# Kernel tuning notes

Measured on AMD Instinct MI355X. Metric: run time of the kernel, lower is better.

## Reference

```python
import jax, jax.numpy as jnp
import numpy as np

QK_K = 256      # super-block size
N_SUB = 8       # sub-blocks per super-block
SUB_SIZE = QK_K // N_SUB  # 32
NMAX_4BIT = 15.0


def _quantize_scales_6bit(scales):
    # scales: (B, N_SUB). Quantize to 6-bit grid [0..63] and dequantize; STE for grads.
    s_min = scales.min(axis=-1, keepdims=True)
    s_max = scales.max(axis=-1, keepdims=True)
    s_range = jnp.maximum(s_max - s_min, 1e-8)
    s_int = jnp.clip(jnp.round((scales - s_min) / s_range * 63.0), 0.0, 63.0)
    s_dequant = s_int / 63.0 * s_range + s_min
    return scales + jax.lax.stop_gradient(s_dequant - scales)


def fake_quantize_q4_k_m(weight):
    orig_shape = weight.shape
    w = weight.reshape(-1)
    pad = (-w.size) % QK_K
    if pad:
        w = jnp.concatenate([w, jnp.zeros((pad,), dtype=w.dtype)])
    # (n_blocks, N_SUB, SUB_SIZE)
    w_sub = w.reshape(-1, N_SUB, SUB_SIZE)
    sub_min = jnp.minimum(w_sub.min(axis=-1), 0.0)   # clamp(max=0)
    sub_max = jnpum if False else jnp.maximum(w_sub.max(axis=-1), 0.0)  # clamp(min=0)
    scale_raw = jnp.maximum(sub_max - sub_min, 1e-8) / NMAX_4BIT
    scale = _quantize_scales_6bit(scale_raw)         # (n_blocks, N_SUB)
    # super-block min, rounded through fp16 with STE
    super_min_raw = sub_min.min(axis=-1, keepdims=True)  # (n_blocks, 1)
    super_min_f16 = super_min_raw.astype(jnp.float16).astype(w.dtype)
    super_min = super_min_raw + jax.lax.stop_gradient(super_min_f16 - super_min_raw)
    adj_min = sub_min - super_min                    # (n_blocks, N_SUB)
    scale_bc = jnp.maximum(scale, 1e-8)[..., None]   # (n_blocks, N_SUB, 1)
    w_int = (w_sub - super_min[..., None] - adj_min[..., None]) / scale_bc
    w_int = jnp.clip(jnp.round(w_int), 0.0, NMAX_4BIT)
    w_dequant = w_int * scale_bc + adj_min[..., None] + super_min[..., None]
    w_out = w_sub + jax.lax.stop_gradient(w_dequant - w_sub)  # STE
    w_flat = w_out.reshape(-1)
    if pad:
        w_flat = w_flat[:-pad]
    return w_flat.reshape(orig_shape)


def setup_inputs() -> dict:
    key = jax.random.key(0)
    k1, k2, k3 = jax.random.split(key, 3)
    x = jax.random.normal(k1, (2, 2048, 4096), dtype=jnp.float32)
    weight = jax.random.normal(k2, (4096, 4096), dtype=jnp.float32) * 0.02
    bias = jax.random.normal(k3, (4096,), dtype=jnp.float32)
    return {"x": x, "weight": weight, "bias": bias}


def reference(x, weight, bias):
    # _qmode = True path: fake-quantize weight to Q4_K_M grid, then dense linear.
    fq_weight = fake_quantize_q4_k_m(weight)
    return jnp.einsum('bsd,od->bso', x, fq_weight) + bias
```

## Files before the change

### kernel.cpp

```cpp
#include <hip/hip_runtime.h>
#include <hip/hip_bf16.h>
#include <hip/hip_fp16.h>


typedef __attribute__((ext_vector_type(8))) short bf16x8;
typedef __attribute__((ext_vector_type(8))) unsigned short ushort8;
typedef __attribute__((ext_vector_type(4))) float f32x4;

__device__ __forceinline__ unsigned short f2bf(float f) {
  unsigned int u = __float_as_uint(f);
  u += 0x7fffu + ((u >> 16) & 1u);
  return (unsigned short)(u >> 16);
}

__global__ __launch_bounds__(256) void prep_kernel(
    const float* __restrict__ x, unsigned short* __restrict__ xb,
    const float* __restrict__ w, unsigned short* __restrict__ wq,
    int castBlocks) {
  if ((int)blockIdx.x < castBlocks) {
    const size_t i = ((size_t)blockIdx.x * 256 + threadIdx.x) * 8;
    const float4 a = *(const float4*)(x + i);
    const float4 b = *(const float4*)(x + i + 4);
    ushort8 o = {f2bf(a.x), f2bf(a.y), f2bf(a.z), f2bf(a.w),
                 f2bf(b.x), f2bf(b.y), f2bf(b.z), f2bf(b.w)};
    *(ushort8*)(xb + i) = o;
    return;
  }
  const int qb   = blockIdx.x - castBlocks;
  const int lane = threadIdx.x & 63;
  const int wv   = threadIdx.x >> 6;
  const size_t base = (((size_t)qb * 4 + wv) * 256) + (size_t)lane * 4;
  const float4 v = *(const float4*)(w + base);

  float mn = fminf(fminf(v.x, v.y), fminf(v.z, v.w));
  float mx = fmaxf(fmaxf(v.x, v.y), fmaxf(v.z, v.w));
#pragma unroll
  for (int off = 1; off <= 4; off <<= 1) {
    mn = fminf(mn, __shfl_xor(mn, off));
    mx = fmaxf(mx, __shfl_xor(mx, off));
  }
  const float sub_min = fminf(mn, 0.0f);
  const float sub_max = fmaxf(mx, 0.0f);
  const float scale_raw = fmaxf(sub_max - sub_min, 1e-8f) / 15.0f;

  float smn = scale_raw, smx = scale_raw, supermin = sub_min;
#pragma unroll
  for (int off = 8; off <= 32; off <<= 1) {
    smn = fminf(smn, __shfl_xor(smn, off));
    smx = fmaxf(smx, __shfl_xor(smx, off));
    supermin = fminf(supermin, __shfl_xor(supermin, off));
  }
  const float s_range = fmaxf(smx - smn, 1e-8f);
  float s_int = rintf((scale_raw - smn) / s_range * 63.0f);
  s_int = fminf(fmaxf(s_int, 0.0f), 63.0f);
  float scale = s_int / 63.0f * s_range + smn;
  scale = fmaxf(scale, 1e-8f);
  const float inv_scale = 1.0f / scale;

  const float sm  = __half2float(__float2half(supermin));
  const float adj = sub_min - sm;

  float e[4] = {v.x, v.y, v.z, v.w};
  ushort4 o;
  unsigned short* op = (unsigned short*)&o;
#pragma unroll
  for (int k = 0; k < 4; ++k) {
    const float t = (e[k] - sm) - adj;
    float qv = rintf(t * inv_scale);
    qv = fminf(fmaxf(qv, 0.0f), 15.0f);
    op[k] = f2bf((qv * scale + adj) + sm);
  }
  *(ushort4*)(wq + base) = o;
}

#define BM 256
#define BN 128
#define BK 64

__device__ __forceinline__ void async_cp16(void* lds, const void* g) {
  __builtin_amdgcn_global_load_lds(
      (__attribute__((address_space(1))) void*)(void*)g,
      (__attribute__((address_space(3))) void*)lds, 16, 0, 0);
}

__global__ __launch_bounds__(256, 2) void gemm_bt_kernel(
    const unsigned short* __restrict__ A,
    const unsigned short* __restrict__ B,
    const float* __restrict__ bias,
    float* __restrict__ C,
    int M, int N, int K) {
  __shared__ unsigned short lds_a[BM * BK];
  __shared__ unsigned short lds_b[BN * BK];

  const int tid  = threadIdx.x;
  const int lane = tid & 63;
  const int wv   = tid >> 6;
  const int wm   = wv >> 1;
  const int wn   = wv & 1;
  const int bx   = blockIdx.x;
  const int by   = blockIdx.y;

  const int rloc = tid >> 3;
  const int csw  = (tid & 7) ^ (rloc & 7);
  const int koff = csw * 8;

  const unsigned short* gA[8];
  const unsigned short* gB[4];
#pragma unroll
  for (int j = 0; j < 8; ++j)
    gA[j] = A + (size_t)(by * BM + j * 32 + rloc) * K + koff;
#pragma unroll
  for (int j = 0; j < 4; ++j)
    gB[j] = B + (size_t)(bx * BN + j * 32 + rloc) * K + koff;

  f32x4 acc[8][4] = {};

  const int arow   = wm * 128 + (lane & 15);
  const int brow   = wn * 64 + (lane & 15);
  const int kslot0 = (((lane >> 4) ^ (lane & 7))) * 8;
  const int kslot1 = kslot0 ^ 32;

  for (int k0 = 0; k0 < K; k0 += BK) {
#pragma unroll
    for (int j = 0; j < 8; ++j)
      async_cp16(lds_a + j * 2048 + tid * 8, gA[j] + k0);
#pragma unroll
    for (int j = 0; j < 4; ++j)
      async_cp16(lds_b + j * 2048 + tid * 8, gB[j] + k0);
    __syncthreads();

#pragma unroll
    for (int h = 0; h < 2; ++h) {
      const int ks = h ? kslot1 : kslot0;
      bf16x8 af[8], bfr[4];
#pragma unroll
      for (int i = 0; i < 8; ++i)
        af[i] = *(const bf16x8*)(lds_a + (arow + i * 16) * BK + ks);
#pragma unroll
      for (int j = 0; j < 4; ++j)
        bfr[j] = *(const bf16x8*)(lds_b + (brow + j * 16) * BK + ks);

#pragma unroll
      for (int i = 0; i < 8; ++i)
#pragma unroll
        for (int j = 0; j < 4; ++j)
          acc[i][j] = __builtin_amdgcn_mfma_f32_16x16x32_bf16(af[i], bfr[j],
                                                              acc[i][j], 0, 0, 0);
    }
    __syncthreads();
  }

  const int rbase = by * BM + wm * 128 + (lane >> 4) * 4;
  const int cbase = bx * BN + wn * 64 + (lane & 15);
#pragma unroll
  for (int j = 0; j < 4; ++j) {
    const int c = cbase + j * 16;
    const float bv = bias[c];
#pragma unroll
    for (int i = 0; i < 8; ++i) {
#pragma unroll
      for (int r = 0; r < 4; ++r) {
        C[(size_t)(rbase + i * 16 + r) * N + c] = acc[i][j][r] + bv;
      }
    }
  }
}

extern "C" void kernel_launch(void* const* d_in, const int* in_sizes, int n_in,
                              void* d_out, int out_size, void* d_ws, size_t ws_size,
                              hipStream_t stream) {
  const float* x    = (const float*)d_in[0];
  const float* w    = (const float*)d_in[1];
  const float* bias = (const float*)d_in[2];
  float* out = (float*)d_out;

  const long long xn = in_sizes[0];
  const long long wn = in_sizes[1];
  const int N = in_sizes[2];
  const int K = (int)(wn / N);
  const int M = (int)(xn / K);

  unsigned short* xb = (unsigned short*)d_ws;
  unsigned short* wb = xb + (size_t)M * K;

  const int castBlocks  = (int)(xn / (256 * 8));
  const int quantBlocks = (int)(wn / (256 * 4));
  prep_kernel<<<castBlocks + quantBlocks, 256, 0, stream>>>(x, xb, w, wb,
                                                            castBlocks);
  gemm_bt_kernel<<<dim3(N / BN, M / BM), 256, 0, stream>>>(xb, wb, bias, out,
                                                           M, N, K);
}
```

Measured before the change: 289.0 us.

## Double-buffer A tile in LDS and load B fragments directly from global

The A tile is double-buffered in LDS, with the next K-step prefetched asynchronously while the current one is computed, which removes one barrier per iteration. B fragments are now read straight from global memory into registers instead of being staged through LDS. The grid is transposed so that consecutive blocks walk along M and share the same B columns. This aims to overlap global loads with MFMA work and to cut LDS traffic, but the direct B loads are strided per-lane 16-byte reads whose latency is not hidden and may be poorly coalesced.

```diff
diff --git a/kernel.cpp b/kernel.cpp
--- a/kernel.cpp
+++ b/kernel.cpp
@@ -89,65 +89,66 @@
     const float* __restrict__ bias,
     float* __restrict__ C,
     int M, int N, int K) {
-  __shared__ unsigned short lds_a[BM * BK];
-  __shared__ unsigned short lds_b[BN * BK];
+  __shared__ unsigned short lds_a[2][BM * BK];
 
   const int tid  = threadIdx.x;
   const int lane = tid & 63;
   const int wv   = tid >> 6;
   const int wm   = wv >> 1;
   const int wn   = wv & 1;
-  const int bx   = blockIdx.x;
-  const int by   = blockIdx.y;
+  const int by   = blockIdx.x;
+  const int bx   = blockIdx.y;
 
   const int rloc = tid >> 3;
   const int csw  = (tid & 7) ^ (rloc & 7);
-  const int koff = csw * 8;
+  const unsigned short* gA = A + (size_t)(by * BM + rloc) * K + csw * 8;
 
-  const unsigned short* gA[8];
-  const unsigned short* gB[4];
-#pragma unroll
-  for (int j = 0; j < 8; ++j)
-    gA[j] = A + (size_t)(by * BM + j * 32 + rloc) * K + koff;
-#pragma unroll
-  for (int j = 0; j < 4; ++j)
-    gB[j] = B + (size_t)(bx * BN + j * 32 + rloc) * K + koff;
+  const unsigned short* bp =
+      B + (size_t)(bx * BN + wn * 64 + (lane & 15)) * K + (lane >> 4) * 8;
 
   f32x4 acc[8][4] = {};
 
   const int arow   = wm * 128 + (lane & 15);
-  const int brow   = wn * 64 + (lane & 15);
   const int kslot0 = (((lane >> 4) ^ (lane & 7))) * 8;
   const int kslot1 = kslot0 ^ 32;
 
+#pragma unroll
+  for (int j = 0; j < 8; ++j)
+    async_cp16(lds_a[0] + j * 2048 + tid * 8, gA + (size_t)j * 32 * K);
+
   for (int k0 = 0; k0 < K; k0 += BK) {
+    const int cur = (k0 >> 6) & 1;
+    __syncthreads();
+    if (k0 + BK < K) {
+      const int nxt = cur ^ 1;
 #pragma unroll
-    for (int j = 0; j < 8; ++j)
-      async_cp16(lds_a + j * 2048 + tid * 8, gA[j] + k0);
+      for (int j = 0; j < 8; ++j)
+        async_cp16(lds_a[nxt] + j * 2048 + tid * 8,
+                   gA + (size_t)j * 32 * K + (k0 + BK));
+    }
+
+    bf16x8 bfr[2][4];
 #pragma unroll
-    for (int j = 0; j < 4; ++j)
-      async_cp16(lds_b + j * 2048 + tid * 8, gB[j] + k0);
-    __syncthreads();
+    for (int h = 0; h < 2; ++h)
+#pragma unroll
+      for (int jt = 0; jt < 4; ++jt)
+        bfr[h][jt] = *(const bf16x8*)(bp + (size_t)jt * 16 * K + k0 + h * 32);
 
 #pragma unroll
     for (int h = 0; h < 2; ++h) {
       const int ks = h ? kslot1 : kslot0;
-      bf16x8 af[8], bfr[4];
+      bf16x8 af[8];
 #pragma unroll
       for (int i = 0; i < 8; ++i)
-        af[i] = *(const bf16x8*)(lds_a + (arow + i * 16) * BK + ks);
-#pragma unroll
-      for (int j = 0; j < 4; ++j)
-        bfr[j] = *(const bf16x8*)(lds_b + (brow + j * 16) * BK + ks);
+        af[i] = *(const bf16x8*)(lds_a[cur] + (arow + i * 16) * BK + ks);
 
 #pragma unroll
       for (int i = 0; i < 8; ++i)
 #pragma unroll
         for (int j = 0; j < 4; ++j)
-          acc[i][j] = __builtin_amdgcn_mfma_f32_16x16x32_bf16(af[i], bfr[j],
-                                                              acc[i][j], 0, 0, 0);
+          acc[i][j] = __builtin_amdgcn_mfma_f32_16x16x32_bf16(
+              af[i], bfr[h][j], acc[i][j], 0, 0, 0);
     }
-    __syncthreads();
   }
 
   const int rbase = by * BM + wm * 128 + (lane >> 4) * 4;
@@ -187,6 +188,6 @@
   const int quantBlocks = (int)(wn / (256 * 4));
   prep_kernel<<<castBlocks + quantBlocks, 256, 0, stream>>>(x, xb, w, wb,
                                                             castBlocks);
-  gemm_bt_kernel<<<dim3(N / BN, M / BM), 256, 0, stream>>>(xb, wb, bias, out,
+  gemm_bt_kernel<<<dim3(M / BM, N / BN), 256, 0, stream>>>(xb, wb, bias, out,
                                                            M, N, K);
 }
```

After: 342.8 us. 18.7% more time.
